# Performance work log

Measured on AMD Instinct MI355X. Metric: run time of the kernel, lower is better.

The kernel has to match this reference:

```python
import jax, jax.numpy as jnp
import numpy as np
import math

B, T, D, H = 16, 512, 1024, 16
DK = D // H
MAX_LEN = 512          # RelativePositionBias default
LOCAL_WINDOW = 128


def setup_inputs() -> dict:
    key = jax.random.key(0)
    ks = jax.random.split(key, 6)
    x = jax.random.normal(ks[0], (B, T, D), dtype=jnp.float32)
    Wqkv = jax.random.normal(ks[1], (D, 3 * D), dtype=jnp.float32) * 0.02
    bqkv = jnp.zeros((3 * D,), dtype=jnp.float32)
    Wo = jax.random.normal(ks[2], (D, D), dtype=jnp.float32) * 0.02
    bo = jnp.zeros((D,), dtype=jnp.float32)
    rel_table = jax.random.normal(ks[3], (2 * MAX_LEN - 1, H), dtype=jnp.float32) * 0.02
    return {"x": x, "Wqkv": Wqkv, "bqkv": bqkv, "Wo": Wo, "bo": bo, "rel_table": rel_table}


def reference(x, Wqkv, bqkv, Wo, bo, rel_table):
    # QKV projection: [B,T,3D]
    qkv = x @ Wqkv + bqkv
    q, k, v = jnp.split(qkv, 3, axis=-1)
    # [B,T,D] -> [B,H,T,DK]
    def to_heads(t):
        return t.reshape(B, T, H, DK).transpose(0, 2, 1, 3)
    q, k, v = to_heads(q), to_heads(k), to_heads(v)

    # scaled dot-product scores: [B,H,T,T]
    scores = jnp.einsum('bhqd,bhkd->bhqk', q, k) / math.sqrt(DK)

    # relative position bias: dist[i,j] = j - i, clipped index in [0, 2*max_len-2]
    r = jnp.arange(T)
    idx = (r[None, :] - r[:, None]) + (MAX_LEN - 1)   # [T,T]
    bias = rel_table[idx]                              # [T,T,H]
    scores = scores + bias.transpose(2, 0, 1)[None]    # [1,H,T,T]

    # local window mask: keep j in [i-w, i+w]
    keep = jnp.abs(r[:, None] - r[None, :]) <= LOCAL_WINDOW  # [T,T]
    scores = jnp.where(keep[None, None], scores, -jnp.inf)

    attn = jax.nn.softmax(scores, axis=-1)
    ctx = jnp.einsum('bhqk,bhkd->bhqd', attn, v)       # [B,H,T,DK]
    ctx = ctx.transpose(0, 2, 1, 3).reshape(B, T, D)
    out = ctx @ Wo + bo
    return (out, attn)
```

## Files before the change

### kernel.cpp

```cpp
#include <hip/hip_runtime.h>
#include <math.h>

typedef unsigned short ushort_t;
typedef __bf16 bf16x8 __attribute__((ext_vector_type(8)));
typedef float f32x4 __attribute__((ext_vector_type(4)));
typedef ushort_t u16x8 __attribute__((ext_vector_type(8)));

#define BB 16
#define TT 512
#define DD 1024
#define HH 16
#define DKK 64
#define WIN 128
#define MAXLEN 512

#define TILE_M 64
#define JSPAN 320
#define NCHUNK 5

#define BK 32
#define TBUF (128 * BK)
#define BUFU (4 * TBUF)
#define KSTEPS (DD / BK)

#define ALS 72

#define GLOAD16(g, l)                                                                              \
    __builtin_amdgcn_global_load_lds((const __attribute__((address_space(1))) unsigned int*)(g),   \
                                     (__attribute__((address_space(3))) unsigned int*)(l), 16, 0, 0)

__device__ __forceinline__ ushort_t f2bf(float f) {
    union { float f; unsigned u; } x; x.f = f;
    unsigned r = x.u + 0x7fffu + ((x.u >> 16) & 1u);
    return (ushort_t)(r >> 16);
}
__device__ __forceinline__ float bf2f(ushort_t h) {
    union { unsigned u; float f; } x; x.u = ((unsigned)h) << 16;
    return x.f;
}

__device__ __forceinline__ int swi(int row, int col) {
    return row * ALS + (col ^ (((row >> 3) & 7) << 3));
}

__global__ __launch_bounds__(256) void conv_split(const float* __restrict__ src,
                                                  ushort_t* __restrict__ hi,
                                                  ushort_t* __restrict__ lo, int n4)
{
    const int i = blockIdx.x * 256 + threadIdx.x;
    if (i >= n4) return;
    float4 vf = ((const float4*)src)[i];
    ushort_t h0 = f2bf(vf.x), h1 = f2bf(vf.y), h2 = f2bf(vf.z), h3 = f2bf(vf.w);
    ushort4 hv = make_ushort4(h0, h1, h2, h3);
    ushort4 lv = make_ushort4(f2bf(vf.x - bf2f(h0)), f2bf(vf.y - bf2f(h1)),
                              f2bf(vf.z - bf2f(h2)), f2bf(vf.w - bf2f(h3)));
    ((ushort4*)hi)[i] = hv;
    ((ushort4*)lo)[i] = lv;
}

__global__ __launch_bounds__(256) void conv_split_T(const float* __restrict__ W,
                                                    ushort_t* __restrict__ hiT,
                                                    ushort_t* __restrict__ loT,
                                                    int K, int N)
{
    __shared__ ushort_t th[32][33], tl[32][33];
    const int n0 = blockIdx.x * 32, k0 = blockIdx.y * 32;
    const int tid = threadIdx.x;
    const int r = tid >> 3, c4 = (tid & 7) * 4;
    float4 vf = *(const float4*)&W[(size_t)(k0 + r) * N + n0 + c4];
    float vv[4] = {vf.x, vf.y, vf.z, vf.w};
#pragma unroll
    for (int j = 0; j < 4; ++j) {
        ushort_t h = f2bf(vv[j]);
        th[r][c4 + j] = h;
        tl[r][c4 + j] = f2bf(vv[j] - bf2f(h));
    }
    __syncthreads();
    ushort4 oh = make_ushort4(th[c4 + 0][r], th[c4 + 1][r], th[c4 + 2][r], th[c4 + 3][r]);
    ushort4 ol = make_ushort4(tl[c4 + 0][r], tl[c4 + 1][r], tl[c4 + 2][r], tl[c4 + 3][r]);
    *(ushort4*)&hiT[(size_t)(n0 + r) * K + k0 + c4] = oh;
    *(ushort4*)&loT[(size_t)(n0 + r) * K + k0 + c4] = ol;
}

__device__ __forceinline__ void mfma_mainloop(const ushort_t* __restrict__ Ah,
                                              const ushort_t* __restrict__ Al,
                                              const ushort_t* __restrict__ Bh,
                                              const ushort_t* __restrict__ Bl,
                                              int m0, int n0,
                                              ushort_t* smem, f32x4 (&acc)[4][4])
{
    const int tid = threadIdx.x;
    const int lane = tid & 63;
    const int w = tid >> 6;
    const int wm = (w >> 1) * 64, wn = (w & 1) * 64;
    const int c16 = lane & 15;
    const int quad = lane >> 4;

    const int lrow = lane >> 2, lq = lane & 3;
    const int r0 = w * 32, r1 = w * 32 + 16;
    const int row0 = r0 + lrow, row1 = r1 + lrow;
    const int qd0 = lq ^ ((row0 >> 1) & 3);
    const int qd1 = lq ^ ((row1 >> 1) & 3);
    const size_t a0 = (size_t)(m0 + row0) * DD + qd0 * 8;
    const size_t a1 = (size_t)(m0 + row1) * DD + qd1 * 8;
    const size_t b0 = (size_t)(n0 + row0) * DD + qd0 * 8;
    const size_t b1 = (size_t)(n0 + row1) * DD + qd1 * 8;

    auto STAGE = [&](int buf, int k0) {
        ushort_t* s_ = smem + buf * BUFU;
        GLOAD16(Ah + a0 + k0, (char*)s_ + r0 * 64);
        GLOAD16(Ah + a1 + k0, (char*)s_ + r1 * 64);
        GLOAD16(Al + a0 + k0, (char*)(s_ + TBUF) + r0 * 64);
        GLOAD16(Al + a1 + k0, (char*)(s_ + TBUF) + r1 * 64);
        GLOAD16(Bh + b0 + k0, (char*)(s_ + 2 * TBUF) + r0 * 64);
        GLOAD16(Bh + b1 + k0, (char*)(s_ + 2 * TBUF) + r1 * 64);
        GLOAD16(Bl + b0 + k0, (char*)(s_ + 3 * TBUF) + r0 * 64);
        GLOAD16(Bl + b1 + k0, (char*)(s_ + 3 * TBUF) + r1 * 64);
    };

    int aoff[4], boff[4];
#pragma unroll
    for (int mt = 0; mt < 4; ++mt) {
        const int row = wm + mt * 16 + c16;
        aoff[mt] = row * BK + ((quad ^ ((row >> 1) & 3)) * 8);
    }
#pragma unroll
    for (int nt = 0; nt < 4; ++nt) {
        const int row = wn + nt * 16 + c16;
        boff[nt] = row * BK + ((quad ^ ((row >> 1) & 3)) * 8);
    }

    STAGE(0, 0);
    for (int t = 0; t < KSTEPS; ++t) {
        const int cur = t & 1;
        if (t + 1 < KSTEPS) {
            STAGE(cur ^ 1, (t + 1) * BK);
            asm volatile("s_waitcnt vmcnt(8)" ::: "memory");
        } else {
            asm volatile("s_waitcnt vmcnt(0)" ::: "memory");
        }
        __builtin_amdgcn_sched_barrier(0);
        __builtin_amdgcn_s_barrier();

        const ushort_t* sAh = smem + cur * BUFU;
        const ushort_t* sAl = sAh + TBUF;
        const ushort_t* sBh = sAh + 2 * TBUF;
        const ushort_t* sBl = sAh + 3 * TBUF;
        bf16x8 ah[4], al[4];
#pragma unroll
        for (int mt = 0; mt < 4; ++mt) {
            ah[mt] = *(const bf16x8*)&sAh[aoff[mt]];
            al[mt] = *(const bf16x8*)&sAl[aoff[mt]];
        }
#pragma unroll
        for (int nt = 0; nt < 4; ++nt) {
            bf16x8 bh = *(const bf16x8*)&sBh[boff[nt]];
            bf16x8 bl = *(const bf16x8*)&sBl[boff[nt]];
#pragma unroll
            for (int mt = 0; mt < 4; ++mt) {
                acc[mt][nt] = __builtin_amdgcn_mfma_f32_16x16x32_bf16(ah[mt], bh, acc[mt][nt], 0, 0, 0);
                acc[mt][nt] = __builtin_amdgcn_mfma_f32_16x16x32_bf16(al[mt], bh, acc[mt][nt], 0, 0, 0);
                acc[mt][nt] = __builtin_amdgcn_mfma_f32_16x16x32_bf16(ah[mt], bl, acc[mt][nt], 0, 0, 0);
            }
        }
        __builtin_amdgcn_sched_barrier(0);
        __builtin_amdgcn_s_barrier();
    }
}

__global__ __launch_bounds__(256) void qkv_mfma(const ushort_t* __restrict__ xh,
                                                const ushort_t* __restrict__ xl,
                                                const ushort_t* __restrict__ wh,
                                                const ushort_t* __restrict__ wl,
                                                const float* __restrict__ bias,
                                                ushort_t* __restrict__ qh,
                                                ushort_t* __restrict__ ql,
                                                ushort_t* __restrict__ kh,
                                                ushort_t* __restrict__ kl,
                                                ushort_t* __restrict__ vh,
                                                ushort_t* __restrict__ vl)
{
    __shared__ ushort_t smem[2 * BUFU];
    f32x4 acc[4][4] = {};
    const int bid = blockIdx.x;
    const int swz = (bid & 7) * 192 + (bid >> 3);
    const int n0 = (swz % 24) * 128;
    const int m0 = (swz / 24) * 128;
    mfma_mainloop(xh, xl, wh, wl, m0, n0, smem, acc);

    const int tid = threadIdx.x, lane = tid & 63, w = tid >> 6;
    const int wm = (w >> 1) * 64, wn = (w & 1) * 64;
    const int c16 = lane & 15, rq = (lane >> 4) * 4;
#pragma unroll
    for (int mt = 0; mt < 4; ++mt)
#pragma unroll
        for (int nt = 0; nt < 4; ++nt)
#pragma unroll
            for (int r = 0; r < 4; ++r) {
                const int m = m0 + wm + mt * 16 + rq + r;
                const int n = n0 + wn + nt * 16 + c16;
                const float val = acc[mt][nt][r] + bias[n];
                const int bidx = m >> 9, t = m & (TT - 1);
                const int sel = n >> 10, d = n & (DD - 1);
                const int hd = d >> 6, dk = d & (DKK - 1);
                ushort_t* dsth = (sel == 0) ? qh : (sel == 1) ? kh : vh;
                ushort_t* dstl = (sel == 0) ? ql : (sel == 1) ? kl : vl;
                const size_t base = ((((size_t)bidx * HH + hd) * TT + t) * DKK) + dk;
                const ushort_t hi = f2bf(val);
                dsth[base] = hi;
                dstl[base] = f2bf(val - bf2f(hi));
            }
}

__global__ __launch_bounds__(256) void out_mfma(const ushort_t* __restrict__ ah,
                                                const ushort_t* __restrict__ al,
                                                const ushort_t* __restrict__ wh,
                                                const ushort_t* __restrict__ wl,
                                                const float* __restrict__ bias,
                                                float* __restrict__ out)
{
    __shared__ ushort_t smem[2 * BUFU];
    f32x4 acc[4][4] = {};
    const int bid = blockIdx.x;
    const int swz = (bid & 7) * 64 + (bid >> 3);
    const int n0 = (swz & 7) * 128;
    const int m0 = (swz >> 3) * 128;
    mfma_mainloop(ah, al, wh, wl, m0, n0, smem, acc);

    const int tid = threadIdx.x, lane = tid & 63, w = tid >> 6;
    const int wm = (w >> 1) * 64, wn = (w & 1) * 64;
    const int c16 = lane & 15, rq = (lane >> 4) * 4;
#pragma unroll
    for (int mt = 0; mt < 4; ++mt)
#pragma unroll
        for (int nt = 0; nt < 4; ++nt)
#pragma unroll
            for (int r = 0; r < 4; ++r) {
                const int m = m0 + wm + mt * 16 + rq + r;
                const int n = n0 + wn + nt * 16 + c16;
                out[(size_t)m * DD + n] = acc[mt][nt][r] + bias[n];
            }
}

__global__ __launch_bounds__(512) void attn_fused(const ushort_t* __restrict__ qh_g,
                                                  const ushort_t* __restrict__ ql_g,
                                                  const ushort_t* __restrict__ kh_g,
                                                  const ushort_t* __restrict__ kl_g,
                                                  const ushort_t* __restrict__ vh_g,
                                                  const ushort_t* __restrict__ vl_g,
                                                  const float* __restrict__ rel,
                                                  float* __restrict__ attn_out,
                                                  ushort_t* __restrict__ cxh,
                                                  ushort_t* __restrict__ cxl)
{
    const int gid = blockIdx.x;
    const int u = gid >> 6, rem = gid & 63;
    const int it = rem >> 3;
    const int bh_idx = u * 8 + (rem & 7);
    const int h = bh_idx & 15, b = bh_idx >> 4;
    const int i0 = it * TILE_M;
    int jbase = i0 - WIN; if (jbase < 0) jbase = 0; if (jbase > TT - JSPAN) jbase = TT - JSPAN;

    const int tid = threadIdx.x;
    const int lane = tid & 63, w = tid >> 6;
    const int c16 = lane & 15, quad = lane >> 4, rq = quad * 4;
    const int wmh = (w >> 2) * 32;
    const int wnq = (w & 3) * 16;

    __shared__ ushort_t sA0[64 * ALS], sA1[64 * ALS];
    __shared__ ushort_t sB0[64 * ALS], sB1[64 * ALS];
    __shared__ float bias_s[1024];
    __shared__ float stats0[256], stats1[256];

    const size_t bh = (size_t)b * HH + h;
    const ushort_t* qhp = qh_g + (bh * TT + i0) * DKK;
    const ushort_t* qlp = ql_g + (bh * TT + i0) * DKK;
    const ushort_t* khp = kh_g + bh * TT * DKK;
    const ushort_t* klp = kl_g + bh * TT * DKK;
    const ushort_t* vhp = vh_g + bh * TT * DKK;
    const ushort_t* vlp = vl_g + bh * TT * DKK;
    float* arow = attn_out + (bh * TT + i0) * TT;

    {
        const float4 z = make_float4(0.f, 0.f, 0.f, 0.f);
        for (int idx = tid; idx < TILE_M * 48; idx += 512) {
            const int r  = idx / 48;
            const int c4 = idx - r * 48;
            const int col = (c4 * 4 < jbase) ? c4 * 4 : c4 * 4 + JSPAN;
            *(float4*)&arow[(size_t)r * TT + col] = z;
        }
    }
    for (int idx = tid; idx < 2 * MAXLEN - 1; idx += 512)
        bias_s[idx] = rel[(size_t)idx * HH + h];

    const int srow = tid >> 3, spart = (tid & 7) * 8;
    *(u16x8*)&sA0[swi(srow, spart)] = *(const u16x8*)&qhp[(size_t)srow * DKK + spart];
    *(u16x8*)&sA1[swi(srow, spart)] = *(const u16x8*)&qlp[(size_t)srow * DKK + spart];

    float s[NCHUNK][2][4];
#pragma unroll
    for (int c = 0; c < NCHUNK; ++c) {
        {
            const size_t g = (size_t)(jbase + c * 64 + srow) * DKK + spart;
            *(u16x8*)&sB0[swi(srow, spart)] = *(const u16x8*)&khp[g];
            *(u16x8*)&sB1[swi(srow, spart)] = *(const u16x8*)&klp[g];
        }
        __syncthreads();
        f32x4 sacc[2] = {};
#pragma unroll
        for (int kk = 0; kk < 2; ++kk) {
            const int ku = kk * 32 + quad * 8;
            const bf16x8 kbh = *(const bf16x8*)&sB0[swi(wnq + c16, ku)];
            const bf16x8 kbl = *(const bf16x8*)&sB1[swi(wnq + c16, ku)];
#pragma unroll
            for (int mt = 0; mt < 2; ++mt) {
                const bf16x8 qah = *(const bf16x8*)&sA0[swi(wmh + mt * 16 + c16, ku)];
                const bf16x8 qal = *(const bf16x8*)&sA1[swi(wmh + mt * 16 + c16, ku)];
                sacc[mt] = __builtin_amdgcn_mfma_f32_16x16x32_bf16(qah, kbh, sacc[mt], 0, 0, 0);
                sacc[mt] = __builtin_amdgcn_mfma_f32_16x16x32_bf16(qal, kbh, sacc[mt], 0, 0, 0);
                sacc[mt] = __builtin_amdgcn_mfma_f32_16x16x32_bf16(qah, kbl, sacc[mt], 0, 0, 0);
            }
        }
        __syncthreads();
#pragma unroll
        for (int mt = 0; mt < 2; ++mt)
#pragma unroll
            for (int r = 0; r < 4; ++r) {
                const int i = i0 + wmh + mt * 16 + rq + r;
                const int j = jbase + c * 64 + wnq + c16;
                const int d = j - i;
                const float val = sacc[mt][r] * 0.125f + bias_s[d + MAXLEN - 1];
                s[c][mt][r] = (d >= -WIN && d <= WIN) ? val : -INFINITY;
            }
    }

    float mrow[2][4];
#pragma unroll
    for (int mt = 0; mt < 2; ++mt)
#pragma unroll
        for (int r = 0; r < 4; ++r) {
            float m = s[0][mt][r];
#pragma unroll
            for (int c = 1; c < NCHUNK; ++c) m = fmaxf(m, s[c][mt][r]);
            mrow[mt][r] = m;
        }
#pragma unroll
    for (int off = 1; off < 16; off <<= 1)
#pragma unroll
        for (int mt = 0; mt < 2; ++mt)
#pragma unroll
            for (int r = 0; r < 4; ++r)
                mrow[mt][r] = fmaxf(mrow[mt][r], __shfl_xor(mrow[mt][r], off));
    if (c16 == 0) {
#pragma unroll
        for (int mt = 0; mt < 2; ++mt)
#pragma unroll
            for (int r = 0; r < 4; ++r)
                stats0[(wmh + mt * 16 + rq + r) * 4 + (w & 3)] = mrow[mt][r];
    }
    __syncthreads();
#pragma unroll
    for (int mt = 0; mt < 2; ++mt)
#pragma unroll
        for (int r = 0; r < 4; ++r) {
            const f32x4 q4 = *(const f32x4*)&stats0[(wmh + mt * 16 + rq + r) * 4];
            mrow[mt][r] = fmaxf(fmaxf(q4[0], q4[1]), fmaxf(q4[2], q4[3]));
        }
    float srow_[2][4];
#pragma unroll
    for (int mt = 0; mt < 2; ++mt)
#pragma unroll
        for (int r = 0; r < 4; ++r) srow_[mt][r] = 0.f;
#pragma unroll
    for (int c = 0; c < NCHUNK; ++c)
#pragma unroll
        for (int mt = 0; mt < 2; ++mt)
#pragma unroll
            for (int r = 0; r < 4; ++r) {
                const float e = __expf(s[c][mt][r] - mrow[mt][r]);
                s[c][mt][r] = e;
                srow_[mt][r] += e;
            }
#pragma unroll
    for (int off = 1; off < 16; off <<= 1)
#pragma unroll
        for (int mt = 0; mt < 2; ++mt)
#pragma unroll
            for (int r = 0; r < 4; ++r)
                srow_[mt][r] += __shfl_xor(srow_[mt][r], off);
    if (c16 == 0) {
#pragma unroll
        for (int mt = 0; mt < 2; ++mt)
#pragma unroll
            for (int r = 0; r < 4; ++r)
                stats1[(wmh + mt * 16 + rq + r) * 4 + (w & 3)] = srow_[mt][r];
    }
    __syncthreads();
    float inv[2][4];
#pragma unroll
    for (int mt = 0; mt < 2; ++mt)
#pragma unroll
        for (int r = 0; r < 4; ++r) {
            const f32x4 q4 = *(const f32x4*)&stats1[(wmh + mt * 16 + rq + r) * 4];
            inv[mt][r] = 1.0f / (q4[0] + q4[1] + q4[2] + q4[3]);
        }

    f32x4 oacc[2] = {};
#pragma unroll
    for (int c = 0; c < NCHUNK; ++c) {
        if (c > 0) __syncthreads();
#pragma unroll
        for (int mt = 0; mt < 2; ++mt)
#pragma unroll
            for (int r = 0; r < 4; ++r) {
                const int i = wmh + mt * 16 + rq + r;
                const float p = s[c][mt][r] * inv[mt][r];
                arow[(size_t)i * TT + jbase + c * 64 + wnq + c16] = p;
                const ushort_t ph = f2bf(p);
                const int col = (wnq + c16) ^ (((i >> 3) & 7) << 3);
                sA0[i * ALS + col] = ph;
                sA1[i * ALS + col] = f2bf(p - bf2f(ph));
            }
        {
            const int jr = tid >> 3, dkb = (tid & 7) * 8;
            const size_t g = (size_t)(jbase + c * 64 + jr) * DKK + dkb;
            const u16x8 v0 = *(const u16x8*)&vhp[g];
            const u16x8 v1 = *(const u16x8*)&vlp[g];
#pragma unroll
            for (int e = 0; e < 8; ++e) {
                const int dk = dkb + e;
                const int idx = dk * ALS + (jr ^ (((dk >> 3) & 7) << 3));
                sB0[idx] = v0[e];
                sB1[idx] = v1[e];
            }
        }
        __syncthreads();
#pragma unroll
        for (int kk = 0; kk < 2; ++kk) {
            const int ku = kk * 32 + quad * 8;
            const bf16x8 vbh = *(const bf16x8*)&sB0[swi(wnq + c16, ku)];
            const bf16x8 vbl = *(const bf16x8*)&sB1[swi(wnq + c16, ku)];
#pragma unroll
            for (int mt = 0; mt < 2; ++mt) {
                const bf16x8 pah = *(const bf16x8*)&sA0[swi(wmh + mt * 16 + c16, ku)];
                const bf16x8 pal = *(const bf16x8*)&sA1[swi(wmh + mt * 16 + c16, ku)];
                oacc[mt] = __builtin_amdgcn_mfma_f32_16x16x32_bf16(pah, vbh, oacc[mt], 0, 0, 0);
                oacc[mt] = __builtin_amdgcn_mfma_f32_16x16x32_bf16(pal, vbh, oacc[mt], 0, 0, 0);
                oacc[mt] = __builtin_amdgcn_mfma_f32_16x16x32_bf16(pah, vbl, oacc[mt], 0, 0, 0);
            }
        }
    }

#pragma unroll
    for (int mt = 0; mt < 2; ++mt)
#pragma unroll
        for (int r = 0; r < 4; ++r) {
            const float val = oacc[mt][r];
            const int i = wmh + mt * 16 + rq + r;
            const int dk = wnq + c16;
            const ushort_t hh2 = f2bf(val);
            const size_t off = (((size_t)b * TT + i0 + i) * HH + h) * DKK + dk;
            cxh[off] = hh2;
            cxl[off] = f2bf(val - bf2f(hh2));
        }
}

extern "C" void kernel_launch(void* const* d_in, const int* in_sizes, int n_in,
                              void* d_out, int out_size, void* d_ws, size_t ws_size,
                              hipStream_t stream)
{
    const float* x    = (const float*)d_in[0];
    const float* Wqkv = (const float*)d_in[1];
    const float* bqkv = (const float*)d_in[2];
    const float* Wo   = (const float*)d_in[3];
    const float* bo   = (const float*)d_in[4];
    const float* rel  = (const float*)d_in[5];

    float* out  = (float*)d_out;
    float* attn = out + (size_t)BB * TT * DD;

    const size_t per = (size_t)BB * HH * TT * DKK;
    ushort_t* qh = (ushort_t*)d_ws;
    ushort_t* ql = qh + per;
    ushort_t* kh = ql + per;
    ushort_t* kl = kh + per;
    ushort_t* vh = kl + per;
    ushort_t* vl = vh + per;
    ushort_t* xh = vl + per;
    ushort_t* xl = xh + per;
    ushort_t* Wqh = xl + per;
    ushort_t* Wql = Wqh + (size_t)DD * 3 * DD;
    ushort_t* cxh = xh;
    ushort_t* cxl = xl;
    ushort_t* Woh = vh;
    ushort_t* Wol = Woh + (size_t)DD * DD;

    const int n4x = BB * TT * DD / 4;

    conv_split<<<dim3((n4x + 255) / 256), 256, 0, stream>>>(x, xh, xl, n4x);
    conv_split_T<<<dim3(3 * DD / 32, DD / 32), 256, 0, stream>>>(Wqkv, Wqh, Wql, DD, 3 * DD);
    qkv_mfma<<<dim3(1536), 256, 0, stream>>>(xh, xl, Wqh, Wql, bqkv, qh, ql, kh, kl, vh, vl);
    attn_fused<<<dim3(2048), 512, 0, stream>>>(qh, ql, kh, kl, vh, vl, rel, attn, cxh, cxl);
    conv_split_T<<<dim3(DD / 32, DD / 32), 256, 0, stream>>>(Wo, Woh, Wol, DD, DD);
    out_mfma<<<dim3(512), 256, 0, stream>>>(cxh, cxl, Woh, Wol, bo, out);
}
```

Before: 651.4 us.

## Split attention blocks into 32-row halves and register-prefetch next K/V chunks

```diff
diff --git a/kernel.cpp b/kernel.cpp
--- a/kernel.cpp
+++ b/kernel.cpp
@@ -242,7 +242,7 @@
             }
 }
 
-__global__ __launch_bounds__(512) void attn_fused(const ushort_t* __restrict__ qh_g,
+__global__ __launch_bounds__(256) void attn_fused(const ushort_t* __restrict__ qh_g,
                                                   const ushort_t* __restrict__ ql_g,
                                                   const ushort_t* __restrict__ kh_g,
                                                   const ushort_t* __restrict__ kl_g,
@@ -254,56 +254,74 @@
                                                   ushort_t* __restrict__ cxl)
 {
     const int gid = blockIdx.x;
-    const int u = gid >> 6, rem = gid & 63;
-    const int it = rem >> 3;
-    const int bh_idx = u * 8 + (rem & 7);
+    const int x = gid & 7;
+    const int v = (gid >> 3) & 15;
+    const int u = gid >> 7;
+    const int it = v >> 1, mh = v & 1;
+    const int bh_idx = u * 8 + x;
     const int h = bh_idx & 15, b = bh_idx >> 4;
     const int i0 = it * TILE_M;
     int jbase = i0 - WIN; if (jbase < 0) jbase = 0; if (jbase > TT - JSPAN) jbase = TT - JSPAN;
+    const int irow0 = i0 + mh * 32;
 
     const int tid = threadIdx.x;
     const int lane = tid & 63, w = tid >> 6;
     const int c16 = lane & 15, quad = lane >> 4, rq = quad * 4;
-    const int wmh = (w >> 2) * 32;
-    const int wnq = (w & 3) * 16;
-
-    __shared__ ushort_t sA0[64 * ALS], sA1[64 * ALS];
+    const int wnq = w * 16;
+
+    __shared__ ushort_t sA0[32 * ALS], sA1[32 * ALS];
     __shared__ ushort_t sB0[64 * ALS], sB1[64 * ALS];
-    __shared__ float bias_s[1024];
-    __shared__ float stats0[256], stats1[256];
+    __shared__ float bias_s[260];
+    __shared__ float stats0[128], stats1[128];
 
     const size_t bh = (size_t)b * HH + h;
-    const ushort_t* qhp = qh_g + (bh * TT + i0) * DKK;
-    const ushort_t* qlp = ql_g + (bh * TT + i0) * DKK;
+    const ushort_t* qhp = qh_g + (bh * TT + irow0) * DKK;
+    const ushort_t* qlp = ql_g + (bh * TT + irow0) * DKK;
     const ushort_t* khp = kh_g + bh * TT * DKK;
     const ushort_t* klp = kl_g + bh * TT * DKK;
     const ushort_t* vhp = vh_g + bh * TT * DKK;
     const ushort_t* vlp = vl_g + bh * TT * DKK;
-    float* arow = attn_out + (bh * TT + i0) * TT;
+    float* arow = attn_out + (bh * TT + irow0) * TT;
+
+    const int srow = tid >> 3, spart = (tid & 7) * 8;
+
+    u16x8 kpre[2][2];
+#pragma unroll
+    for (int ii = 0; ii < 2; ++ii) {
+        const size_t g = (size_t)(jbase + ii * 32 + srow) * DKK + spart;
+        kpre[ii][0] = *(const u16x8*)&khp[g];
+        kpre[ii][1] = *(const u16x8*)&klp[g];
+    }
 
     {
         const float4 z = make_float4(0.f, 0.f, 0.f, 0.f);
-        for (int idx = tid; idx < TILE_M * 48; idx += 512) {
+        for (int idx = tid; idx < 32 * 48; idx += 256) {
             const int r  = idx / 48;
             const int c4 = idx - r * 48;
             const int col = (c4 * 4 < jbase) ? c4 * 4 : c4 * 4 + JSPAN;
             *(float4*)&arow[(size_t)r * TT + col] = z;
         }
     }
-    for (int idx = tid; idx < 2 * MAXLEN - 1; idx += 512)
-        bias_s[idx] = rel[(size_t)idx * HH + h];
-
-    const int srow = tid >> 3, spart = (tid & 7) * 8;
+    if (tid < 257) bias_s[tid] = rel[(size_t)(tid + MAXLEN - 1 - 128) * HH + h];
+
     *(u16x8*)&sA0[swi(srow, spart)] = *(const u16x8*)&qhp[(size_t)srow * DKK + spart];
     *(u16x8*)&sA1[swi(srow, spart)] = *(const u16x8*)&qlp[(size_t)srow * DKK + spart];
 
-    float s[NCHUNK][2][4];
+    float s[NCHUNK][8];
 #pragma unroll
     for (int c = 0; c < NCHUNK; ++c) {
-        {
-            const size_t g = (size_t)(jbase + c * 64 + srow) * DKK + spart;
-            *(u16x8*)&sB0[swi(srow, spart)] = *(const u16x8*)&khp[g];
-            *(u16x8*)&sB1[swi(srow, spart)] = *(const u16x8*)&klp[g];
+#pragma unroll
+        for (int ii = 0; ii < 2; ++ii) {
+            *(u16x8*)&sB0[swi(ii * 32 + srow, spart)] = kpre[ii][0];
+            *(u16x8*)&sB1[swi(ii * 32 + srow, spart)] = kpre[ii][1];
+        }
+        if (c + 1 < NCHUNK) {
+#pragma unroll
+            for (int ii = 0; ii < 2; ++ii) {
+                const size_t g = (size_t)(jbase + (c + 1) * 64 + ii * 32 + srow) * DKK + spart;
+                kpre[ii][0] = *(const u16x8*)&khp[g];
+                kpre[ii][1] = *(const u16x8*)&klp[g];
+            }
         }
         __syncthreads();
         f32x4 sacc[2] = {};
@@ -314,8 +332,8 @@
             const bf16x8 kbl = *(const bf16x8*)&sB1[swi(wnq + c16, ku)];
 #pragma unroll
             for (int mt = 0; mt < 2; ++mt) {
-                const bf16x8 qah = *(const bf16x8*)&sA0[swi(wmh + mt * 16 + c16, ku)];
-                const bf16x8 qal = *(const bf16x8*)&sA1[swi(wmh + mt * 16 + c16, ku)];
+                const bf16x8 qah = *(const bf16x8*)&sA0[swi(mt * 16 + c16, ku)];
+                const bf16x8 qal = *(const bf16x8*)&sA1[swi(mt * 16 + c16, ku)];
                 sacc[mt] = __builtin_amdgcn_mfma_f32_16x16x32_bf16(qah, kbh, sacc[mt], 0, 0, 0);
                 sacc[mt] = __builtin_amdgcn_mfma_f32_16x16x32_bf16(qal, kbh, sacc[mt], 0, 0, 0);
                 sacc[mt] = __builtin_amdgcn_mfma_f32_16x16x32_bf16(qah, kbl, sacc[mt], 0, 0, 0);
@@ -326,11 +344,12 @@
         for (int mt = 0; mt < 2; ++mt)
 #pragma unroll
             for (int r = 0; r < 4; ++r) {
-                const int i = i0 + wmh + mt * 16 + rq + r;
+                const int i = irow0 + mt * 16 + rq + r;
                 const int j = jbase + c * 64 + wnq + c16;
                 const int d = j - i;
-                const float val = sacc[mt][r] * 0.125f + bias_s[d + MAXLEN - 1];
-                s[c][mt][r] = (d >= -WIN && d <= WIN) ? val : -INFINITY;
+                const int bi = (d < -128) ? -128 : (d > 128 ? 128 : d);
+                const float val = sacc[mt][r] * 0.125f + bias_s[bi + 128];
+                s[c][mt * 4 + r] = (d >= -WIN && d <= WIN) ? val : -INFINITY;
             }
     }
 
@@ -339,9 +358,9 @@
     for (int mt = 0; mt < 2; ++mt)
 #pragma unroll
         for (int r = 0; r < 4; ++r) {
-            float m = s[0][mt][r];
-#pragma unroll
-            for (int c = 1; c < NCHUNK; ++c) m = fmaxf(m, s[c][mt][r]);
+            float m = s[0][mt * 4 + r];
+#pragma unroll
+            for (int c = 1; c < NCHUNK; ++c) m = fmaxf(m, s[c][mt * 4 + r]);
             mrow[mt][r] = m;
         }
 #pragma unroll
@@ -356,14 +375,14 @@
         for (int mt = 0; mt < 2; ++mt)
 #pragma unroll
             for (int r = 0; r < 4; ++r)
-                stats0[(wmh + mt * 16 + rq + r) * 4 + (w & 3)] = mrow[mt][r];
+                stats0[(mt * 16 + rq + r) * 4 + w] = mrow[mt][r];
     }
     __syncthreads();
 #pragma unroll
     for (int mt = 0; mt < 2; ++mt)
 #pragma unroll
         for (int r = 0; r < 4; ++r) {
-            const f32x4 q4 = *(const f32x4*)&stats0[(wmh + mt * 16 + rq + r) * 4];
+            const f32x4 q4 = *(const f32x4*)&stats0[(mt * 16 + rq + r) * 4];
             mrow[mt][r] = fmaxf(fmaxf(q4[0], q4[1]), fmaxf(q4[2], q4[3]));
         }
     float srow_[2][4];
@@ -377,8 +396,8 @@
         for (int mt = 0; mt < 2; ++mt)
 #pragma unroll
             for (int r = 0; r < 4; ++r) {
-                const float e = __expf(s[c][mt][r] - mrow[mt][r]);
-                s[c][mt][r] = e;
+                const float e = __expf(s[c][mt * 4 + r] - mrow[mt][r]);
+                s[c][mt * 4 + r] = e;
                 srow_[mt][r] += e;
             }
 #pragma unroll
@@ -393,7 +412,7 @@
         for (int mt = 0; mt < 2; ++mt)
 #pragma unroll
             for (int r = 0; r < 4; ++r)
-                stats1[(wmh + mt * 16 + rq + r) * 4 + (w & 3)] = srow_[mt][r];
+                stats1[(mt * 16 + rq + r) * 4 + w] = srow_[mt][r];
     }
     __syncthreads();
     float inv[2][4];
@@ -401,9 +420,17 @@
     for (int mt = 0; mt < 2; ++mt)
 #pragma unroll
         for (int r = 0; r < 4; ++r) {
-            const f32x4 q4 = *(const f32x4*)&stats1[(wmh + mt * 16 + rq + r) * 4];
+            const f32x4 q4 = *(const f32x4*)&stats1[(mt * 16 + rq + r) * 4];
             inv[mt][r] = 1.0f / (q4[0] + q4[1] + q4[2] + q4[3]);
         }
+
+    u16x8 vpre[2][2];
+#pragma unroll
+    for (int ii = 0; ii < 2; ++ii) {
+        const size_t g = (size_t)(jbase + ii * 32 + srow) * DKK + spart;
+        vpre[ii][0] = *(const u16x8*)&vhp[g];
+        vpre[ii][1] = *(const u16x8*)&vlp[g];
+    }
 
     f32x4 oacc[2] = {};
 #pragma unroll
@@ -413,25 +440,31 @@
         for (int mt = 0; mt < 2; ++mt)
 #pragma unroll
             for (int r = 0; r < 4; ++r) {
-                const int i = wmh + mt * 16 + rq + r;
-                const float p = s[c][mt][r] * inv[mt][r];
+                const int i = mt * 16 + rq + r;
+                const float p = s[c][mt * 4 + r] * inv[mt][r];
                 arow[(size_t)i * TT + jbase + c * 64 + wnq + c16] = p;
                 const ushort_t ph = f2bf(p);
                 const int col = (wnq + c16) ^ (((i >> 3) & 7) << 3);
                 sA0[i * ALS + col] = ph;
                 sA1[i * ALS + col] = f2bf(p - bf2f(ph));
             }
-        {
-            const int jr = tid >> 3, dkb = (tid & 7) * 8;
-            const size_t g = (size_t)(jbase + c * 64 + jr) * DKK + dkb;
-            const u16x8 v0 = *(const u16x8*)&vhp[g];
-            const u16x8 v1 = *(const u16x8*)&vlp[g];
+#pragma unroll
+        for (int ii = 0; ii < 2; ++ii) {
+            const int jr = ii * 32 + srow;
 #pragma unroll
             for (int e = 0; e < 8; ++e) {
-                const int dk = dkb + e;
+                const int dk = spart + e;
                 const int idx = dk * ALS + (jr ^ (((dk >> 3) & 7) << 3));
-                sB0[idx] = v0[e];
-                sB1[idx] = v1[e];
+                sB0[idx] = vpre[ii][0][e];
+                sB1[idx] = vpre[ii][1][e];
+            }
+        }
+        if (c + 1 < NCHUNK) {
+#pragma unroll
+            for (int ii = 0; ii < 2; ++ii) {
+                const size_t g = (size_t)(jbase + (c + 1) * 64 + ii * 32 + srow) * DKK + spart;
+                vpre[ii][0] = *(const u16x8*)&vhp[g];
+                vpre[ii][1] = *(const u16x8*)&vlp[g];
             }
         }
         __syncthreads();
@@ -442,8 +475,8 @@
             const bf16x8 vbl = *(const bf16x8*)&sB1[swi(wnq + c16, ku)];
 #pragma unroll
             for (int mt = 0; mt < 2; ++mt) {
-                const bf16x8 pah = *(const bf16x8*)&sA0[swi(wmh + mt * 16 + c16, ku)];
-                const bf16x8 pal = *(const bf16x8*)&sA1[swi(wmh + mt * 16 + c16, ku)];
+                const bf16x8 pah = *(const bf16x8*)&sA0[swi(mt * 16 + c16, ku)];
+                const bf16x8 pal = *(const bf16x8*)&sA1[swi(mt * 16 + c16, ku)];
                 oacc[mt] = __builtin_amdgcn_mfma_f32_16x16x32_bf16(pah, vbh, oacc[mt], 0, 0, 0);
                 oacc[mt] = __builtin_amdgcn_mfma_f32_16x16x32_bf16(pal, vbh, oacc[mt], 0, 0, 0);
                 oacc[mt] = __builtin_amdgcn_mfma_f32_16x16x32_bf16(pah, vbl, oacc[mt], 0, 0, 0);
@@ -456,10 +489,10 @@
 #pragma unroll
         for (int r = 0; r < 4; ++r) {
             const float val = oacc[mt][r];
-            const int i = wmh + mt * 16 + rq + r;
+            const int i = mt * 16 + rq + r;
             const int dk = wnq + c16;
             const ushort_t hh2 = f2bf(val);
-            const size_t off = (((size_t)b * TT + i0 + i) * HH + h) * DKK + dk;
+            const size_t off = (((size_t)b * TT + irow0 + i) * HH + h) * DKK + dk;
             cxh[off] = hh2;
             cxl[off] = f2bf(val - bf2f(hh2));
         }
@@ -500,7 +533,7 @@
     conv_split<<<dim3((n4x + 255) / 256), 256, 0, stream>>>(x, xh, xl, n4x);
     conv_split_T<<<dim3(3 * DD / 32, DD / 32), 256, 0, stream>>>(Wqkv, Wqh, Wql, DD, 3 * DD);
     qkv_mfma<<<dim3(1536), 256, 0, stream>>>(xh, xl, Wqh, Wql, bqkv, qh, ql, kh, kl, vh, vl);
-    attn_fused<<<dim3(2048), 512, 0, stream>>>(qh, ql, kh, kl, vh, vl, rel, attn, cxh, cxl);
+    attn_fused<<<dim3(4096), 256, 0, stream>>>(qh, ql, kh, kl, vh, vl, rel, attn, cxh, cxl);
     conv_split_T<<<dim3(DD / 32, DD / 32), 256, 0, stream>>>(Wo, Woh, Wol, DD, DD);
     out_mfma<<<dim3(512), 256, 0, stream>>>(cxh, cxl, Woh, Wol, bo, out);
 }
```

Result: faster. 625.7 us (-3.9%).
